# Optimization experiments

Measured on AMD Instinct MI355X. Metric: run time of the kernel, lower is better.

Reference implementation:

```python
import jax, jax.numpy as jnp
import numpy as np

B, S, D, H, HD, F = 8, 1024, 512, 8, 64, 2048
EPS = 1e-6

def rmsnorm(x, w):
    var = jnp.mean(x * x, axis=-1, keepdims=True)
    return w * (x * jax.lax.rsqrt(var + EPS))

def setup_inputs() -> dict:
    key = jax.random.key(0)
    ks = jax.random.split(key, 10)
    sd = 512 ** -0.5
    return {
        "primals_1": jax.random.normal(ks[0], (D, D), jnp.float32) * sd,
        "primals_2": jax.random.normal(ks[1], (D, D), jnp.float32) * sd,
        "primals_3": jax.random.normal(ks[2], (D, D), jnp.float32) * sd,
        "primals_4": jax.random.normal(ks[3], (D, D), jnp.float32) * sd,
        "primals_5": jax.random.uniform(ks[4], (D,), jnp.float32, 0.5, 1.5),
        "primals_6": jax.random.normal(ks[5], (F, D), jnp.float32) * sd,
        "primals_7": jax.random.normal(ks[6], (D, F), jnp.float32) * (F ** -0.5),
        "primals_8": jax.random.uniform(ks[7], (D,), jnp.float32, 0.5, 1.5),
        "primals_9": jax.random.normal(ks[8], (B, S, D), jnp.float32),
        "primals_10": jax.random.normal(ks[9], (B, H, S, S), jnp.float32) * 0.1,
    }

def reference(primals_1, primals_2, primals_3, primals_4, primals_5,
              primals_6, primals_7, primals_8, primals_9, primals_10):
    x = primals_9
    # --- self-attention sublayer ---
    h = rmsnorm(x, primals_5)                      # [B,S,D]
    # T5: no 1/sqrt(head_dim) scaling
    q = (h @ primals_3.T).reshape(B, S, H, HD).transpose(0, 2, 1, 3)  # [B,H,S,HD]
    k = (h @ primals_1.T).reshape(B, S, H, HD).transpose(0, 2, 1, 3)
    v = (h @ primals_4.T).reshape(B, S, H, HD).transpose(0, 2, 1, 3)
    scores = jnp.einsum('bhqd,bhkd->bhqk', q, k) + primals_10        # [B,H,S,S]
    attn = jax.nn.softmax(scores, axis=-1)
    ctx = jnp.einsum('bhqk,bhkd->bhqd', attn, v)                     # [B,H,S,HD]
    ctx = ctx.transpose(0, 2, 1, 3).reshape(B, S, D)
    x = x + ctx @ primals_2.T                       # residual add_1
    # --- FFN sublayer ---
    h2 = rmsnorm(x, primals_8)
    ff = jax.nn.relu(h2 @ primals_6.T)              # [B,S,F]
    out = x + ff @ primals_7.T                      # add_3
    return out
```

## Files before the change

### kernel.cpp

```cpp
#include <hip/hip_runtime.h>

#define B_ 8
#define S_ 1024
#define D_ 512
#define H_ 8
#define HD_ 64
#define F_ 2048

typedef unsigned short u16;
typedef unsigned int u32;
typedef __attribute__((ext_vector_type(8))) short bf16x8;
typedef __attribute__((ext_vector_type(4))) float f32x4;

__device__ __forceinline__ float bf2f(u16 u) {
  union { unsigned int i; float f; } v; v.i = ((unsigned int)u) << 16; return v.f;
}
__device__ __forceinline__ u16 f2bf(float f) {
  union { float f; unsigned int i; } v; v.f = f;
  unsigned int r = v.i + 0x7fffu + ((v.i >> 16) & 1u);
  return (u16)(r >> 16);
}

__device__ __forceinline__ void gl2lds16(const u16* g, u16* lds) {
  __builtin_amdgcn_global_load_lds(
      (const __attribute__((address_space(1))) unsigned int*)g,
      (__attribute__((address_space(3))) unsigned int*)lds, 16, 0, 0);
}

__global__ __launch_bounds__(256) void cvt_w_k(const float* __restrict__ wq, const float* __restrict__ wk,
                                               const float* __restrict__ wv, const float* __restrict__ wo,
                                               const float* __restrict__ wf1, const float* __restrict__ wf2,
                                               u16* __restrict__ dst) {
  size_t gid = (size_t)blockIdx.x * 256 + threadIdx.x;
  size_t e0 = gid * 4;
  const float* src; size_t loc;
  if      (e0 <  262144) { src = wq;  loc = e0; }
  else if (e0 <  524288) { src = wk;  loc = e0 -  262144; }
  else if (e0 <  786432) { src = wv;  loc = e0 -  524288; }
  else if (e0 < 1048576) { src = wo;  loc = e0 -  786432; }
  else if (e0 < 2097152) { src = wf1; loc = e0 - 1048576; }
  else                   { src = wf2; loc = e0 - 2097152; }
  float4 v = *(const float4*)(src + loc);
  ushort4 o; o.x = f2bf(v.x); o.y = f2bf(v.y); o.z = f2bf(v.z); o.w = f2bf(v.w);
  *(ushort4*)(dst + e0) = o;
}

template <int IN_BF16>
__global__ __launch_bounds__(256) void rmsnorm_k(const void* __restrict__ xv,
                                                 const float* __restrict__ w,
                                                 u16* __restrict__ out) {
  int row = blockIdx.x;
  int tid = threadIdx.x;
  float x0, x1;
  if (IN_BF16) {
    u32 v = ((const u32*)((const u16*)xv + (size_t)row * D_))[tid];
    x0 = bf2f((u16)(v & 0xffffu)); x1 = bf2f((u16)(v >> 16));
  } else {
    float2 v = ((const float2*)((const float*)xv + (size_t)row * D_))[tid];
    x0 = v.x; x1 = v.y;
  }
  float s = x0 * x0 + x1 * x1;
#pragma unroll
  for (int off = 32; off >= 1; off >>= 1) s += __shfl_xor(s, off, 64);
  __shared__ float red[4];
  int lane = tid & 63, wid = tid >> 6;
  if (lane == 0) red[wid] = s;
  __syncthreads();
  float tot = red[0] + red[1] + red[2] + red[3];
  float inv = rsqrtf(tot * (1.0f / D_) + 1e-6f);
  float2 wv = ((const float2*)w)[tid];
  u32 o = (u32)f2bf(x0 * inv * wv.x) | ((u32)f2bf(x1 * inv * wv.y) << 16);
  ((u32*)(out + (size_t)row * D_))[tid] = o;
}

template <int RELU, int RMODE, int OF32, int BM>
__global__ __launch_bounds__(256) void gemm_mfma_k(const u16* __restrict__ A,
                                                   const u16* __restrict__ W,
                                                   const void* __restrict__ Rv,
                                                   void* __restrict__ Cv,
                                                   int M, int N, int K) {
  constexpr int MI  = BM / 32;
  constexpr int ACH = BM / 16;
  __shared__ __align__(16) u16 As[BM * 32];
  __shared__ __align__(16) u16 Bs[128 * 32];
  int tid = threadIdx.x;
  int w = tid >> 6, l = tid & 63;
  int quad = l >> 4, l16 = l & 15;
  int m0 = blockIdx.y * BM, n0 = blockIdx.x * 128;
  int wr = (w >> 1) * (BM / 2), wc = (w & 1) * 64;

  int c_sw = (l & 3) ^ ((l >> 2) & 3);
  int r_in = l >> 2;
  int swz = quad ^ (l16 & 3);

  f32x4 acc[MI][4];
#pragma unroll
  for (int i = 0; i < MI; i++)
#pragma unroll
    for (int j = 0; j < 4; j++) acc[i][j] = (f32x4)(0.0f);

  for (int k0 = 0; k0 < K; k0 += 32) {
    __syncthreads();
#pragma unroll
    for (int t = 0; t < (ACH + 8) / 4; t++) {
      int ch = w * ((ACH + 8) / 4) + t;
      const u16* src; u16* dst;
      if (ch < ACH) { src = A + (size_t)(m0 + ch * 16 + r_in) * K;        dst = As + ch * 512; }
      else          { src = W + (size_t)(n0 + (ch - ACH) * 16 + r_in) * K; dst = Bs + (ch - ACH) * 512; }
      gl2lds16(src + k0 + c_sw * 8, dst);
    }
    __syncthreads();
    bf16x8 af[MI], bf[4];
#pragma unroll
    for (int i = 0; i < MI; i++)
      af[i] = *(const bf16x8*)(As + (wr + i * 16 + l16) * 32 + swz * 8);
#pragma unroll
    for (int j = 0; j < 4; j++)
      bf[j] = *(const bf16x8*)(Bs + (wc + j * 16 + l16) * 32 + swz * 8);
#pragma unroll
    for (int i = 0; i < MI; i++)
#pragma unroll
      for (int j = 0; j < 4; j++)
        acc[i][j] = __builtin_amdgcn_mfma_f32_16x16x32_bf16(af[i], bf[j], acc[i][j], 0, 0, 0);
  }

#pragma unroll
  for (int i = 0; i < MI; i++)
#pragma unroll
    for (int r = 0; r < 4; r++) {
      int mrow = m0 + wr + i * 16 + quad * 4 + r;
      size_t base = (size_t)mrow * N + n0 + wc + l16;
#pragma unroll
      for (int j = 0; j < 4; j++) {
        float v = acc[i][j][r];
        if (RELU) v = fmaxf(v, 0.0f);
        if (RMODE == 1) v += ((const float*)Rv)[base + j * 16];
        if (RMODE == 2) v += bf2f(((const u16*)Rv)[base + j * 16]);
        if (OF32) ((float*)Cv)[base + j * 16] = v;
        else      ((u16*)Cv)[base + j * 16]   = f2bf(v);
      }
    }
}

__global__ __launch_bounds__(256) void transpose_v_k(const u16* __restrict__ qkv,
                                                     u16* __restrict__ vt) {
  __shared__ u16 T[64][72];
  int t = threadIdx.x;
  int s0 = blockIdx.x * 64, h = blockIdx.y, b = blockIdx.z;
  int skey = t >> 3, dch = (t & 7) * 8;
  int rot = dch >> 3;
#pragma unroll
  for (int rnd = 0; rnd < 2; rnd++) {
    int s = s0 + skey + rnd * 32;
    bf16x8 vv = *(const bf16x8*)(qkv + ((size_t)(b * S_) + s) * 1536 + 1024 + h * HD_ + dch);
#pragma unroll
    for (int i = 0; i < 8; i++) {
      int ii = (i + rot) & 7;
      T[dch + ii][skey + rnd * 32] = (u16)((short*)&vv)[ii];
    }
  }
  __syncthreads();
  int d = t >> 2, kc = (t & 3) * 16;
  bf16x8 a0 = *(const bf16x8*)(&T[d][kc]);
  bf16x8 a1 = *(const bf16x8*)(&T[d][kc + 8]);
  u16* dst = vt + ((size_t)(b * H_ + h) * HD_ + d) * S_ + s0 + kc;
  *(bf16x8*)dst       = a0;
  *(bf16x8*)(dst + 8) = a1;
}


__device__ __forceinline__ void attn_stage(const u16* __restrict__ qkv,
                                           const u16* __restrict__ vt,
                                           u16* kvbuf, int b, int h, int kt,
                                           int w, int lane) {
#pragma unroll
  for (int i = 0; i < 2; i++) {
    int slot = w * 2 + i;
    int bufid = slot >> 2;
    int qq = slot & 3;
    int srow = qq * 16 + (lane >> 2);
    int slc = (lane & 3) ^ (srow & 3);
    const u16* src;
    if (bufid == 0)
      src = qkv + ((size_t)(b * S_) + kt + srow) * 1536 + 512 + h * HD_ + slc * 8;
    else if (bufid == 1)
      src = qkv + ((size_t)(b * S_) + kt + srow) * 1536 + 544 + h * HD_ + slc * 8;
    else if (bufid == 2)
      src = vt + ((size_t)((b * H_ + h) * HD_) + srow) * S_ + kt + slc * 8;
    else
      src = vt + ((size_t)((b * H_ + h) * HD_) + srow) * S_ + kt + 32 + slc * 8;
    gl2lds16(src, kvbuf + bufid * 2048 + qq * 512);
  }
}

__global__ __launch_bounds__(512, 4) void attn_v4_k(const u16* __restrict__ qkv,
                                                    const u16* __restrict__ vt,
                                                    const float* __restrict__ bias,
                                                    u16* __restrict__ ctx) {
  int tid = threadIdx.x;
  int w = tid >> 6, lane = tid & 63;
  int quad = lane >> 4, l16 = lane & 15;
  int h = blockIdx.y, b = blockIdx.z;
  int q0 = blockIdx.x * 128;

  __shared__ __align__(16) u16 KV[2][4 * 2048];
  __shared__ __align__(16) u16 Pl[8][16 * 72];

  const u16* qrow = qkv + ((size_t)(b * S_) + q0 + w * 16 + l16) * 1536 + h * HD_;
  bf16x8 qf0 = *(const bf16x8*)(qrow + quad * 8);
  bf16x8 qf1 = *(const bf16x8*)(qrow + 32 + quad * 8);

  float mr[4], lr[4];
  f32x4 Oacc[4];
#pragma unroll
  for (int r = 0; r < 4; r++) { mr[r] = -1e30f; lr[r] = 0.0f; }
#pragma unroll
  for (int nt = 0; nt < 4; nt++) Oacc[nt] = (f32x4)(0.0f);

  const float* bpw = bias + ((size_t)((b * H_ + h) * S_) + q0 + w * 16) * S_;

  float bc[4][4], bn[4][4];
#pragma unroll
  for (int r = 0; r < 4; r++) {
    size_t bro = (size_t)(quad * 4 + r) * S_ + l16;
    bc[r][0] = bpw[bro];      bc[r][1] = bpw[bro + 16];
    bc[r][2] = bpw[bro + 32]; bc[r][3] = bpw[bro + 48];
  }

  int cur = 0;
  attn_stage(qkv, vt, &KV[0][0], b, h, 0, w, lane);

  for (int t = 0; t < 16; t++) {
    int kt = t * 64;
    __syncthreads();
    if (t < 15) {
      attn_stage(qkv, vt, &KV[cur ^ 1][0], b, h, kt + 64, w, lane);
#pragma unroll
      for (int r = 0; r < 4; r++) {
        size_t bro = (size_t)(quad * 4 + r) * S_ + kt + 64 + l16;
        bn[r][0] = bpw[bro];      bn[r][1] = bpw[bro + 16];
        bn[r][2] = bpw[bro + 32]; bn[r][3] = bpw[bro + 48];
      }
    }
    const u16* kvb = &KV[cur][0];

    f32x4 sg[4];
    __builtin_amdgcn_s_setprio(1);
#pragma unroll
    for (int g = 0; g < 4; g++) {
      int row = g * 16 + l16;
      int sw = quad ^ (row & 3);
      bf16x8 kf0 = *(const bf16x8*)(kvb + row * 32 + sw * 8);
      bf16x8 kf1 = *(const bf16x8*)(kvb + 2048 + row * 32 + sw * 8);
      f32x4 a = (f32x4)(0.0f);
      a = __builtin_amdgcn_mfma_f32_16x16x32_bf16(qf0, kf0, a, 0, 0, 0);
      a = __builtin_amdgcn_mfma_f32_16x16x32_bf16(qf1, kf1, a, 0, 0, 0);
      sg[g] = a;
    }
    __builtin_amdgcn_s_setprio(0);

#pragma unroll
    for (int r = 0; r < 4; r++) {
      float s0 = sg[0][r] + bc[r][0], s1 = sg[1][r] + bc[r][1];
      float s2 = sg[2][r] + bc[r][2], s3 = sg[3][r] + bc[r][3];
      float t4 = fmaxf(fmaxf(s0, s1), fmaxf(s2, s3));
      t4 = fmaxf(t4, __shfl_xor(t4, 1, 64));
      t4 = fmaxf(t4, __shfl_xor(t4, 2, 64));
      t4 = fmaxf(t4, __shfl_xor(t4, 4, 64));
      t4 = fmaxf(t4, __shfl_xor(t4, 8, 64));
      float mn = fmaxf(mr[r], t4);
      float alpha = __expf(mr[r] - mn);
      float p0 = __expf(s0 - mn), p1 = __expf(s1 - mn);
      float p2 = __expf(s2 - mn), p3 = __expf(s3 - mn);
      float rs = (p0 + p1) + (p2 + p3);
      rs += __shfl_xor(rs, 1, 64);
      rs += __shfl_xor(rs, 2, 64);
      rs += __shfl_xor(rs, 4, 64);
      rs += __shfl_xor(rs, 8, 64);
      lr[r] = lr[r] * alpha + rs;
      mr[r] = mn;
#pragma unroll
      for (int nt = 0; nt < 4; nt++) Oacc[nt][r] *= alpha;
      u16* prow = &Pl[w][(quad * 4 + r) * 72];
      prow[l16]      = f2bf(p0);
      prow[16 + l16] = f2bf(p1);
      prow[32 + l16] = f2bf(p2);
      prow[48 + l16] = f2bf(p3);
    }
    bf16x8 pf0 = *(const bf16x8*)(&Pl[w][l16 * 72 + quad * 8]);
    bf16x8 pf1 = *(const bf16x8*)(&Pl[w][l16 * 72 + 32 + quad * 8]);

    __builtin_amdgcn_s_setprio(1);
#pragma unroll
    for (int nt = 0; nt < 4; nt++) {
      int row = nt * 16 + l16;
      int sw = quad ^ (row & 3);
      bf16x8 vf0 = *(const bf16x8*)(kvb + 4096 + row * 32 + sw * 8);
      bf16x8 vf1 = *(const bf16x8*)(kvb + 6144 + row * 32 + sw * 8);
      Oacc[nt] = __builtin_amdgcn_mfma_f32_16x16x32_bf16(pf0, vf0, Oacc[nt], 0, 0, 0);
      Oacc[nt] = __builtin_amdgcn_mfma_f32_16x16x32_bf16(pf1, vf1, Oacc[nt], 0, 0, 0);
    }
    __builtin_amdgcn_s_setprio(0);

    if (t < 15) {
#pragma unroll
      for (int r = 0; r < 4; r++)
#pragma unroll
        for (int j = 0; j < 4; j++) bc[r][j] = bn[r][j];
    }
    cur ^= 1;
  }

  size_t obase = ((size_t)(b * S_) + q0 + w * 16) * D_ + h * HD_;
#pragma unroll
  for (int r = 0; r < 4; r++) {
    float inv = 1.0f / lr[r];
    int qr = quad * 4 + r;
#pragma unroll
    for (int nt = 0; nt < 4; nt++) {
      ctx[obase + (size_t)qr * D_ + nt * 16 + l16] = f2bf(Oacc[nt][r] * inv);
    }
  }
}

extern "C" void kernel_launch(void* const* d_in, const int* in_sizes, int n_in,
                              void* d_out, int out_size, void* d_ws, size_t ws_size,
                              hipStream_t stream) {
  const float* Wk   = (const float*)d_in[0];
  const float* Wo   = (const float*)d_in[1];
  const float* Wq   = (const float*)d_in[2];
  const float* Wv   = (const float*)d_in[3];
  const float* g1   = (const float*)d_in[4];
  const float* Wf1  = (const float*)d_in[5];
  const float* Wf2  = (const float*)d_in[6];
  const float* g2   = (const float*)d_in[7];
  const float* X    = (const float*)d_in[8];
  const float* bias = (const float*)d_in[9];
  float* out = (float*)d_out;

  const size_t MD = (size_t)B_ * S_ * D_;
  u16* wbf   = (u16*)d_ws;
  u16* Wqkvb = wbf;
  u16* Wob   = wbf +  786432;
  u16* Wf1b  = wbf + 1048576;
  u16* Wf2b  = wbf + 2097152;
  u16* h     = wbf + 3145728;
  u16* qkv   = h + MD;
  u16* vtb   = qkv + 3 * MD;
  u16* ctx   = vtb + MD;
  u16* ff    = ctx + MD;
  u16* x1    = qkv;
  u16* h2    = h;

  dim3 blk(256);
  const int M = B_ * S_;

  cvt_w_k<<<3072, blk, 0, stream>>>(Wq, Wk, Wv, Wo, Wf1, Wf2, wbf);

  rmsnorm_k<0><<<M, blk, 0, stream>>>(X, g1, h);

  dim3 gqkv(1536 / 128, M / 128);
  gemm_mfma_k<0, 0, 0, 128><<<gqkv, blk, 0, stream>>>(h, Wqkvb, nullptr, qkv, M, 1536, D_);

  dim3 gt(S_ / 64, H_, B_);
  transpose_v_k<<<gt, blk, 0, stream>>>(qkv, vtb);

  dim3 ga(S_ / 128, H_, B_);
  attn_v4_k<<<ga, dim3(512), 0, stream>>>(qkv, vtb, bias, ctx);

  dim3 g512(D_ / 128, M / 128);
  gemm_mfma_k<0, 1, 0, 128><<<g512, blk, 0, stream>>>(ctx, Wob, X, x1, M, D_, D_);

  rmsnorm_k<1><<<M, blk, 0, stream>>>(x1, g2, h2);

  dim3 gff1(F_ / 128, M / 128);
  gemm_mfma_k<1, 0, 0, 128><<<gff1, blk, 0, stream>>>(h2, Wf1b, nullptr, ff, M, F_, D_);

  gemm_mfma_k<0, 2, 1, 128><<<g512, blk, 0, stream>>>(ff, Wf2b, x1, out, M, D_, F_);
}
```

Measured before the change: 577.4 us.

## Double-buffer GEMM LDS tiles, add lazy softmax rescale, shrink N=512 GEMM tiles

The GEMM kernel now uses two LDS buffers and issues the global-to-LDS loads for the next K slice before computing on the current one. This removes one barrier per K step and lets memory traffic overlap the MFMA work. The attention kernel skips the cross-lane max reduction and the output rescale whenever every lane's new local max stays within 8 of the running max. Row sums are kept per lane and reduced only once at the end. The two GEMMs with N=512 switch to 64-row tiles to launch more blocks, at the cost of doubling LDS use in the GEMM and relying on implicit waits for the asynchronous LDS loads.

Result: slower. 927.4 us (+60.6%).

```diff
diff --git a/kernel.cpp b/kernel.cpp
--- a/kernel.cpp
+++ b/kernel.cpp
@@ -81,8 +81,9 @@
                                                    int M, int N, int K) {
   constexpr int MI  = BM / 32;
   constexpr int ACH = BM / 16;
-  __shared__ __align__(16) u16 As[BM * 32];
-  __shared__ __align__(16) u16 Bs[128 * 32];
+  constexpr int CPW = (ACH + 8) / 4;
+  __shared__ __align__(16) u16 As[2 * BM * 32];
+  __shared__ __align__(16) u16 Bs[2 * 128 * 32];
   int tid = threadIdx.x;
   int w = tid >> 6, l = tid & 63;
   int quad = l >> 4, l16 = l & 15;
@@ -99,29 +100,37 @@
 #pragma unroll
     for (int j = 0; j < 4; j++) acc[i][j] = (f32x4)(0.0f);
 
+  auto stage = [&](int buf, int k0) {
+#pragma unroll
+    for (int t = 0; t < CPW; t++) {
+      int ch = w * CPW + t;
+      const u16* src; u16* dst;
+      if (ch < ACH) { src = A + (size_t)(m0 + ch * 16 + r_in) * K;         dst = As + buf * (BM * 32) + ch * 512; }
+      else          { src = W + (size_t)(n0 + (ch - ACH) * 16 + r_in) * K; dst = Bs + buf * (128 * 32) + (ch - ACH) * 512; }
+      gl2lds16(src + k0 + c_sw * 8, dst);
+    }
+  };
+
+  stage(0, 0);
+  int cur = 0;
   for (int k0 = 0; k0 < K; k0 += 32) {
     __syncthreads();
-#pragma unroll
-    for (int t = 0; t < (ACH + 8) / 4; t++) {
-      int ch = w * ((ACH + 8) / 4) + t;
-      const u16* src; u16* dst;
-      if (ch < ACH) { src = A + (size_t)(m0 + ch * 16 + r_in) * K;        dst = As + ch * 512; }
-      else          { src = W + (size_t)(n0 + (ch - ACH) * 16 + r_in) * K; dst = Bs + (ch - ACH) * 512; }
-      gl2lds16(src + k0 + c_sw * 8, dst);
-    }
-    __syncthreads();
+    if (k0 + 32 < K) stage(cur ^ 1, k0 + 32);
+    const u16* Asb = As + cur * (BM * 32);
+    const u16* Bsb = Bs + cur * (128 * 32);
     bf16x8 af[MI], bf[4];
 #pragma unroll
     for (int i = 0; i < MI; i++)
-      af[i] = *(const bf16x8*)(As + (wr + i * 16 + l16) * 32 + swz * 8);
+      af[i] = *(const bf16x8*)(Asb + (wr + i * 16 + l16) * 32 + swz * 8);
 #pragma unroll
     for (int j = 0; j < 4; j++)
-      bf[j] = *(const bf16x8*)(Bs + (wc + j * 16 + l16) * 32 + swz * 8);
+      bf[j] = *(const bf16x8*)(Bsb + (wc + j * 16 + l16) * 32 + swz * 8);
 #pragma unroll
     for (int i = 0; i < MI; i++)
 #pragma unroll
       for (int j = 0; j < 4; j++)
         acc[i][j] = __builtin_amdgcn_mfma_f32_16x16x32_bf16(af[i], bf[j], acc[i][j], 0, 0, 0);
+    cur ^= 1;
   }
 
 #pragma unroll
@@ -193,7 +202,7 @@
   }
 }
 
-__global__ __launch_bounds__(512, 4) void attn_v4_k(const u16* __restrict__ qkv,
+__global__ __launch_bounds__(512, 4) void attn_v5_k(const u16* __restrict__ qkv,
                                                     const u16* __restrict__ vt,
                                                     const float* __restrict__ bias,
                                                     u16* __restrict__ ctx) {
@@ -263,29 +272,36 @@
     for (int r = 0; r < 4; r++) {
       float s0 = sg[0][r] + bc[r][0], s1 = sg[1][r] + bc[r][1];
       float s2 = sg[2][r] + bc[r][2], s3 = sg[3][r] + bc[r][3];
-      float t4 = fmaxf(fmaxf(s0, s1), fmaxf(s2, s3));
-      t4 = fmaxf(t4, __shfl_xor(t4, 1, 64));
-      t4 = fmaxf(t4, __shfl_xor(t4, 2, 64));
-      t4 = fmaxf(t4, __shfl_xor(t4, 4, 64));
-      t4 = fmaxf(t4, __shfl_xor(t4, 8, 64));
-      float mn = fmaxf(mr[r], t4);
-      float alpha = __expf(mr[r] - mn);
-      float p0 = __expf(s0 - mn), p1 = __expf(s1 - mn);
-      float p2 = __expf(s2 - mn), p3 = __expf(s3 - mn);
-      float rs = (p0 + p1) + (p2 + p3);
-      rs += __shfl_xor(rs, 1, 64);
-      rs += __shfl_xor(rs, 2, 64);
-      rs += __shfl_xor(rs, 4, 64);
-      rs += __shfl_xor(rs, 8, 64);
-      lr[r] = lr[r] * alpha + rs;
-      mr[r] = mn;
-#pragma unroll
-      for (int nt = 0; nt < 4; nt++) Oacc[nt][r] *= alpha;
+      float lmax = fmaxf(fmaxf(s0, s1), fmaxf(s2, s3));
       u16* prow = &Pl[w][(quad * 4 + r) * 72];
-      prow[l16]      = f2bf(p0);
-      prow[16 + l16] = f2bf(p1);
-      prow[32 + l16] = f2bf(p2);
-      prow[48 + l16] = f2bf(p3);
+      if (__all(lmax - mr[r] <= 8.0f)) {
+        float mn = mr[r];
+        float p0 = __expf(s0 - mn), p1 = __expf(s1 - mn);
+        float p2 = __expf(s2 - mn), p3 = __expf(s3 - mn);
+        lr[r] += (p0 + p1) + (p2 + p3);
+        prow[l16]      = f2bf(p0);
+        prow[16 + l16] = f2bf(p1);
+        prow[32 + l16] = f2bf(p2);
+        prow[48 + l16] = f2bf(p3);
+      } else {
+        float t4 = lmax;
+        t4 = fmaxf(t4, __shfl_xor(t4, 1, 64));
+        t4 = fmaxf(t4, __shfl_xor(t4, 2, 64));
+        t4 = fmaxf(t4, __shfl_xor(t4, 4, 64));
+        t4 = fmaxf(t4, __shfl_xor(t4, 8, 64));
+        float mn = fmaxf(mr[r], t4);
+        float alpha = __expf(mr[r] - mn);
+        float p0 = __expf(s0 - mn), p1 = __expf(s1 - mn);
+        float p2 = __expf(s2 - mn), p3 = __expf(s3 - mn);
+        lr[r] = lr[r] * alpha + (p0 + p1) + (p2 + p3);
+        mr[r] = mn;
+#pragma unroll
+        for (int nt = 0; nt < 4; nt++) Oacc[nt][r] *= alpha;
+        prow[l16]      = f2bf(p0);
+        prow[16 + l16] = f2bf(p1);
+        prow[32 + l16] = f2bf(p2);
+        prow[48 + l16] = f2bf(p3);
+      }
     }
     bf16x8 pf0 = *(const bf16x8*)(&Pl[w][l16 * 72 + quad * 8]);
     bf16x8 pf1 = *(const bf16x8*)(&Pl[w][l16 * 72 + 32 + quad * 8]);
@@ -314,7 +330,12 @@
   size_t obase = ((size_t)(b * S_) + q0 + w * 16) * D_ + h * HD_;
 #pragma unroll
   for (int r = 0; r < 4; r++) {
-    float inv = 1.0f / lr[r];
+    float s = lr[r];
+    s += __shfl_xor(s, 1, 64);
+    s += __shfl_xor(s, 2, 64);
+    s += __shfl_xor(s, 4, 64);
+    s += __shfl_xor(s, 8, 64);
+    float inv = 1.0f / s;
     int qr = quad * 4 + r;
 #pragma unroll
     for (int nt = 0; nt < 4; nt++) {
@@ -366,15 +387,15 @@
   transpose_v_k<<<gt, blk, 0, stream>>>(qkv, vtb);
 
   dim3 ga(S_ / 128, H_, B_);
-  attn_v4_k<<<ga, dim3(512), 0, stream>>>(qkv, vtb, bias, ctx);
-
-  dim3 g512(D_ / 128, M / 128);
-  gemm_mfma_k<0, 1, 0, 128><<<g512, blk, 0, stream>>>(ctx, Wob, X, x1, M, D_, D_);
+  attn_v5_k<<<ga, dim3(512), 0, stream>>>(qkv, vtb, bias, ctx);
+
+  dim3 g512b(D_ / 128, M / 64);
+  gemm_mfma_k<0, 1, 0, 64><<<g512b, blk, 0, stream>>>(ctx, Wob, X, x1, M, D_, D_);
 
   rmsnorm_k<1><<<M, blk, 0, stream>>>(x1, g2, h2);
 
   dim3 gff1(F_ / 128, M / 128);
   gemm_mfma_k<1, 0, 0, 128><<<gff1, blk, 0, stream>>>(h2, Wf1b, nullptr, ff, M, F_, D_);
 
-  gemm_mfma_k<0, 2, 1, 128><<<g512, blk, 0, stream>>>(ff, Wf2b, x1, out, M, D_, F_);
-}
+  gemm_mfma_k<0, 2, 1, 64><<<g512b, blk, 0, stream>>>(ff, Wf2b, x1, out, M, D_, F_);
+}
```
